# Kernel optimization log

Measured on AMD Instinct MI355X. Metric: run time of the kernel, lower is better.

The kernel has to match this reference:

```python
import jax, jax.numpy as jnp
import numpy as np

T, B, D, H = 32, 128, 256, 768
MAX_PONDER = 8
EPS = 0.01


def setup_inputs() -> dict:
    key = jax.random.key(0)
    ks = jax.random.split(key, 6)
    s = 1.0 / np.sqrt(H)
    return {
        "input_": jax.random.normal(ks[0], (T, B, D), jnp.float32),
        "W_ih": jax.random.uniform(ks[1], (H, D + 1), jnp.float32, -s, s),
        "W_hh": jax.random.uniform(ks[2], (H, H), jnp.float32, -s, s),
        "b_ih": jax.random.uniform(ks[3], (H,), jnp.float32, -s, s),
        "b_hh": jax.random.uniform(ks[4], (H,), jnp.float32, -s, s),
        "w_p": jax.random.uniform(ks[5], (H,), jnp.float32, -s, s),
        "b_p": jnp.ones((1,), jnp.float32),  # torch reset_parameters fills ponder bias with 1
    }


def reference(input_, W_ih, W_hh, b_ih, b_hh, w_p, b_p):
    T_, B_, D_ = input_.shape
    H_ = W_hh.shape[0]
    dt = input_.dtype
    hx0 = jnp.zeros((B_, H_), dt)

    def time_step(carry, x_t):
        hx, pcost = carry

        def ponder(c, _):
            hx_i, ah, ahx, sc, spc, mask, flag = c
            # input row with ponder flag (0 on first act step, 1 afterwards)
            x_in = jnp.concatenate([x_t, jnp.full((B_, 1), flag, dt)], axis=1)
            # ponder cost assigned for active rows before update
            spc = jnp.where(mask, -ah, spc)
            hx_new = jnp.tanh(x_in @ W_ih.T + b_ih + hx_i @ W_hh.T + b_hh)
            hx_i = jnp.where(mask[:, None], hx_new, hx_i)
            mf = mask.astype(dt)
            ahx = ahx + mf[:, None] * hx_new  # accum_hx += hx (as in source)
            h = jax.nn.sigmoid(hx_new @ w_p + b_p[0])
            ah2 = ah + mf * h
            p = h - jnp.maximum(ah2 - 1.0, 0.0)
            ahx = ahx + (mf * p)[:, None] * hx_new  # accum_hx += p*hx
            sc = sc + mf
            mask2 = ah2 < (1.0 - EPS)
            return (hx_i, ah2, ahx, sc, spc, mask2, jnp.ones((), dt)), None

        init = (hx,
                jnp.zeros((B_,), dt),           # accum_h
                jnp.zeros((B_, H_), dt),        # accum_hx
                jnp.zeros((B_,), dt),           # step_count
                jnp.zeros((B_,), dt),           # step_ponder_cost
                jnp.ones((B_,), bool),          # selector
                jnp.zeros((), dt))              # flag
        (hx_i, ah, ahx, sc, spc, mask, flag), _ = jax.lax.scan(
            ponder, init, None, length=MAX_PONDER)
        hx_out = ahx / sc[:, None]
        return (hx_out, pcost + spc), (hx_out, sc)

    (hx_last, pcost), (all_hx, steps) = jax.lax.scan(
        time_step, (hx0, jnp.zeros((B_,), dt)), input_)
    # all_hx: [T,B,H], hx: [1,B,H], ponder_cost: [B], ponder_times: [T,B]
    return all_hx, hx_last[None], pcost, steps
```

## Files before the change

### kernel.cpp

```cpp
#include <hip/hip_runtime.h>
#include <math.h>

#define TT 32
#define BB 128
#define DD 256
#define HH 768
#define MAXP 8

#define RG   8
#define RPG  16
#define CB   12
#define CS   64
#define NTH  256
#define NCH  24

#define OFF_LAST  ((size_t)TT * BB * HH)
#define OFF_PCOST (OFF_LAST + (size_t)BB * HH)
#define OFF_STEPS (OFF_PCOST + BB)

#define ASCOPE __HIP_MEMORY_SCOPE_AGENT

typedef __attribute__((ext_vector_type(8))) short s16x8;
typedef __attribute__((ext_vector_type(4))) float f32x4;
typedef unsigned long long ull;

static __device__ __forceinline__ unsigned short f2bf(float f) {
    unsigned u = __float_as_uint(f);
    u = (u + 0x7fffu + ((u >> 16) & 1u)) >> 16;
    return (unsigned short)u;
}
static __device__ __forceinline__ float bf2f(unsigned short h) {
    return __uint_as_float(((unsigned)h) << 16);
}

__launch_bounds__(NTH, 1)
__global__ void act_kernel(const float* __restrict__ x,
                           const float* __restrict__ Wih,
                           const float* __restrict__ Whh,
                           const float* __restrict__ bih,
                           const float* __restrict__ bhh,
                           const float* __restrict__ wpv,
                           const float* __restrict__ bp,
                           float* __restrict__ out,
                           unsigned* __restrict__ flags,
                           ull* __restrict__ hxe)
{
    const int tid  = threadIdx.x;
    const int g    = blockIdx.x & 7;
    const int ib   = blockIdx.x >> 3;
    const int r0   = g * RPG;
    const int c0   = ib * CS;
    const int CT   = tid >> 6;
    const int lane = tid & 63;
    const int am   = lane & 15;
    const int aq   = lane >> 4;

    __shared__ s16x8 A_s[NCH * 64];
    __shared__ s16x8 WB_s[4 * 8 * 64];
    __shared__ s16x8 xA_s[8 * 64];
    __shared__ unsigned short hxn_s[RPG][72];
    __shared__ float zw_s[4][20];
    __shared__ float bias_s[CS], wflag_s[CS];

    s16x8 Breg[NCH];
    {
        const float* wr = Whh + (size_t)(c0 + CT*16 + am) * HH + aq*8;
        for (int ch = 0; ch < NCH; ++ch) {
            float4 a0 = *(const float4*)(wr + ch*32);
            float4 a1 = *(const float4*)(wr + ch*32 + 4);
            union { s16x8 v; unsigned short e[8]; } u;
            u.e[0]=f2bf(a0.x); u.e[1]=f2bf(a0.y); u.e[2]=f2bf(a0.z); u.e[3]=f2bf(a0.w);
            u.e[4]=f2bf(a1.x); u.e[5]=f2bf(a1.y); u.e[6]=f2bf(a1.z); u.e[7]=f2bf(a1.w);
            Breg[ch] = u.v;
        }
    }
    for (int ch = 0; ch < 8; ++ch) {
        const float* wr = Wih + (size_t)(c0 + CT*16 + am) * (DD+1) + ch*32 + aq*8;
        union { s16x8 v; unsigned short e[8]; } u;
        #pragma unroll
        for (int j = 0; j < 8; ++j) u.e[j] = f2bf(wr[j]);
        WB_s[(CT*8 + ch)*64 + lane] = u.v;
    }
    if (tid < CS) {
        bias_s[tid]  = bih[c0+tid] + bhh[c0+tid];
        wflag_s[tid] = Wih[(size_t)(c0+tid)*(DD+1) + DD];
    }
    const float bpr = bp[0];
    float wpreg[48];
    #pragma unroll
    for (int j = 0; j < 6; ++j)
        #pragma unroll
        for (int i = 0; i < 8; ++i)
            wpreg[j*8+i] = wpv[(j*4 + CT)*32 + aq*8 + i];
    {
        s16x8 z8 = {0,0,0,0,0,0,0,0};
        #pragma unroll
        for (int j = 0; j < 6; ++j) A_s[j*NTH + tid] = z8;
    }

    float ahx[48];
    unsigned it = 0;
    float ahR = 0.f, spcR = 0.f, scR = 0.f, pcR = 0.f;
    int   actR = 1;

    float4 xp0, xp1, xp2, xp3;
    {
        const float* xb = x + (size_t)(r0 + am)*DD;
        xp0 = *(const float4*)(xb + CT*32 + aq*8);
        xp1 = *(const float4*)(xb + CT*32 + aq*8 + 4);
        xp2 = *(const float4*)(xb + (4+CT)*32 + aq*8);
        xp3 = *(const float4*)(xb + (4+CT)*32 + aq*8 + 4);
    }
    __syncthreads();

    for (int t = 0; t < TT; ++t) {
        {
            union { s16x8 v; unsigned short e[8]; } u;
            u.e[0]=f2bf(xp0.x); u.e[1]=f2bf(xp0.y); u.e[2]=f2bf(xp0.z); u.e[3]=f2bf(xp0.w);
            u.e[4]=f2bf(xp1.x); u.e[5]=f2bf(xp1.y); u.e[6]=f2bf(xp1.z); u.e[7]=f2bf(xp1.w);
            xA_s[tid] = u.v;
            u.e[0]=f2bf(xp2.x); u.e[1]=f2bf(xp2.y); u.e[2]=f2bf(xp2.z); u.e[3]=f2bf(xp2.w);
            u.e[4]=f2bf(xp3.x); u.e[5]=f2bf(xp3.y); u.e[6]=f2bf(xp3.z); u.e[7]=f2bf(xp3.w);
            xA_s[NTH + tid] = u.v;
        }
        ahR = 0.f; spcR = 0.f; scR = 0.f; actR = 1;
        #pragma unroll
        for (int q = 0; q < 48; ++q) ahx[q] = 0.f;
        __syncthreads();

        f32x4 xi;
        {
            f32x4 a0 = {0.f,0.f,0.f,0.f}, a1 = {0.f,0.f,0.f,0.f};
            #pragma unroll
            for (int ch = 0; ch < 8; ch += 2) {
                a0 = __builtin_amdgcn_mfma_f32_16x16x32_bf16(
                        xA_s[ch*64 + lane],     WB_s[(CT*8 + ch)*64 + lane],     a0, 0,0,0);
                a1 = __builtin_amdgcn_mfma_f32_16x16x32_bf16(
                        xA_s[(ch+1)*64 + lane], WB_s[(CT*8 + ch+1)*64 + lane],   a1, 0,0,0);
            }
            const float bs = bias_s[CT*16 + am];
            xi[0]=a0[0]+a1[0]+bs; xi[1]=a0[1]+a1[1]+bs;
            xi[2]=a0[2]+a1[2]+bs; xi[3]=a0[3]+a1[3]+bs;
        }
        if (t + 1 < TT) {
            const float* xb = x + ((size_t)(t+1)*BB + r0 + am)*DD;
            xp0 = *(const float4*)(xb + CT*32 + aq*8);
            xp1 = *(const float4*)(xb + CT*32 + aq*8 + 4);
            xp2 = *(const float4*)(xb + (4+CT)*32 + aq*8);
            xp3 = *(const float4*)(xb + (4+CT)*32 + aq*8 + 4);
        }

        int pk = 0;
        for (;;) {
            const unsigned par = it & 1u;
            ull* exch = hxe + (size_t)(g*2 + par) * (NCH*64*2);

            f32x4 a0 = xi, a1 = {0.f,0.f,0.f,0.f};
            #pragma unroll
            for (int ch = 0; ch < NCH; ch += 2) {
                a0 = __builtin_amdgcn_mfma_f32_16x16x32_bf16(A_s[ch*64 + lane],     Breg[ch],   a0, 0,0,0);
                a1 = __builtin_amdgcn_mfma_f32_16x16x32_bf16(A_s[(ch+1)*64 + lane], Breg[ch+1], a1, 0,0,0);
            }
            const float fl = pk ? wflag_s[CT*16 + am] : 0.f;
            #pragma unroll
            for (int r = 0; r < 4; ++r)
                hxn_s[aq*4 + r][CT*16 + am] = f2bf(tanhf(a0[r] + a1[r] + fl));
            __syncthreads();

            {
                const int u4  = tid >> 6, l = tid & 63;
                const int chd = u4 >> 1, half = u4 & 1;
                const int pm  = l & 15, pq = l >> 4;
                const ull v = *(const ull*)&hxn_s[pm][chd*32 + pq*8 + half*4];
                __hip_atomic_store(exch + ((size_t)((2*ib + chd)*64 + l)*2 + half),
                                   v, __ATOMIC_RELAXED, ASCOPE);
            }
            ++it;
            __syncthreads();
            if (tid == 0)
                __hip_atomic_store(&flags[g*16 + ib], it, __ATOMIC_RELEASE, ASCOPE);
            if (tid < 64) {
                const unsigned* fa = &flags[g*16 + (tid % 12)];
                unsigned v;
                do { v = __hip_atomic_load(fa, __ATOMIC_RELAXED, ASCOPE); }
                while (!__all((int)(v >= it)));
                __builtin_amdgcn_fence(__ATOMIC_ACQUIRE, "agent");
            }
            __syncthreads();

            ull nlo[6], nhi[6];
            #pragma unroll
            for (int j = 0; j < 6; ++j) {
                ull* src = exch + (size_t)(j*NTH + tid)*2;
                nlo[j] = __hip_atomic_load(src,     __ATOMIC_RELAXED, ASCOPE);
                nhi[j] = __hip_atomic_load(src + 1, __ATOMIC_RELAXED, ASCOPE);
            }

            float zp = 0.f;
            #pragma unroll
            for (int j = 0; j < 6; ++j) {
                const ull lo = nlo[j], hi = nhi[j];
                #pragma unroll
                for (int i = 0; i < 4; ++i) {
                    zp += bf2f((unsigned short)(lo >> (16*i))) * wpreg[j*8 + i];
                    zp += bf2f((unsigned short)(hi >> (16*i))) * wpreg[j*8 + 4 + i];
                }
            }
            zp += __shfl_xor(zp, 16);
            zp += __shfl_xor(zp, 32);
            if (lane < 16) zw_s[CT][lane] = zp;
            __syncthreads();
            const float z = ((zw_s[0][am] + zw_s[1][am]) + zw_s[2][am]) + zw_s[3][am];

            float w1 = 0.f;
            if (actR) {
                const float h = 1.f / (1.f + expf(-(z + bpr)));
                spcR = -ahR;
                const float ah2 = ahR + h;
                const float p = h - fmaxf(ah2 - 1.f, 0.f);
                w1 = 1.f + p;
                scR += 1.f;
                ahR = ah2;
                actR = (ah2 < 0.99f) ? 1 : 0;
            }

            if (w1 != 0.f) {
                #pragma unroll
                for (int j = 0; j < 6; ++j) {
                    const ull lo = nlo[j], hi = nhi[j];
                    #pragma unroll
                    for (int i = 0; i < 4; ++i) {
                        ahx[j*8 + i]     += w1 * bf2f((unsigned short)(lo >> (16*i)));
                        ahx[j*8 + 4 + i] += w1 * bf2f((unsigned short)(hi >> (16*i)));
                    }
                    union { ull u[2]; s16x8 v; } cv; cv.u[0] = lo; cv.u[1] = hi;
                    A_s[j*NTH + tid] = cv.v;
                }
            }
            const int nact = (int)__popcll(__ballot(actR != 0) & 0xFFFFull);
            ++pk;
            __syncthreads();
            if (nact == 0 || pk == MAXP) break;
        }

        pcR += spcR;
        const float inv = 1.f / scR;
        if (ib == 0 && tid < 16) out[OFF_STEPS + (size_t)t*BB + r0 + tid] = scR;
        #pragma unroll
        for (int j = 0; j < 6; ++j) {
            float o[8];
            #pragma unroll
            for (int i = 0; i < 8; ++i) o[i] = ahx[j*8 + i] * inv;
            union { s16x8 v; unsigned short e[8]; } u;
            #pragma unroll
            for (int i = 0; i < 8; ++i) u.e[i] = f2bf(o[i]);
            A_s[j*NTH + tid] = u.v;
            if (ib == 0) {
                float* op = out + ((size_t)t*BB + r0 + am)*HH + (j*4 + CT)*32 + aq*8;
                *(float4*)op       = make_float4(o[0], o[1], o[2], o[3]);
                *(float4*)(op + 4) = make_float4(o[4], o[5], o[6], o[7]);
                if (t == TT-1) {
                    float* lp = out + OFF_LAST + (size_t)(r0 + am)*HH + (j*4 + CT)*32 + aq*8;
                    *(float4*)lp       = make_float4(o[0], o[1], o[2], o[3]);
                    *(float4*)(lp + 4) = make_float4(o[4], o[5], o[6], o[7]);
                }
            }
        }
        __syncthreads();
    }
    if (ib == 0 && tid < 16) out[OFF_PCOST + r0 + tid] = pcR;
}

extern "C" void kernel_launch(void* const* d_in, const int* in_sizes, int n_in,
                              void* d_out, int out_size, void* d_ws, size_t ws_size,
                              hipStream_t stream) {
    const float* x   = (const float*)d_in[0];
    const float* Wih = (const float*)d_in[1];
    const float* Whh = (const float*)d_in[2];
    const float* bih = (const float*)d_in[3];
    const float* bhh = (const float*)d_in[4];
    const float* wpv = (const float*)d_in[5];
    const float* bp  = (const float*)d_in[6];
    float* out = (float*)d_out;

    unsigned* flags = (unsigned*)d_ws;
    ull*      hxe   = (ull*)((char*)d_ws + 4096);

    hipMemsetAsync(d_ws, 0, 4096, stream);
    act_kernel<<<dim3(RG*CB), dim3(NTH), 0, stream>>>(
        x, Wih, Whh, bih, bhh, wpv, bp, out, flags, hxe);
}
```

Baseline: 406.1 us.

## Replace flag barrier with sequence-tagged exchange words for inter-block hidden-state sync

Each 64-bit exchange word now carries three bf16 values plus a 16-bit sequence tag, so consumers poll the data directly until every tag matches the current iteration. This removes the separate release-flag store, the flag spin-wait and a block barrier from every ponder step. A lagging progress counter, checked two iterations back, protects the double-buffered slots from being overwritten early. The cost is 33% more exchange traffic, wider polling loads, and a larger workspace memset.

```diff
diff --git a/kernel.cpp b/kernel.cpp
--- a/kernel.cpp
+++ b/kernel.cpp
@@ -19,6 +19,8 @@
 #define OFF_STEPS (OFF_PCOST + BB)
 
 #define ASCOPE __HIP_MEMORY_SCOPE_AGENT
+
+#define BUF_ULL (RPG * 96 * 3)
 
 typedef __attribute__((ext_vector_type(8))) short s16x8;
 typedef __attribute__((ext_vector_type(4))) float f32x4;
@@ -42,7 +44,7 @@
                            const float* __restrict__ wpv,
                            const float* __restrict__ bp,
                            float* __restrict__ out,
-                           unsigned* __restrict__ flags,
+                           unsigned* __restrict__ progress,
                            ull* __restrict__ hxe)
 {
     const int tid  = threadIdx.x;
@@ -99,9 +101,12 @@
     }
 
     float ahx[48];
-    unsigned it = 0;
+    unsigned it = 1;
     float ahR = 0.f, spcR = 0.f, scR = 0.f, pcR = 0.f;
     int   actR = 1;
+
+    const int wr_r = tid >> 3;
+    const int wr_o = tid & 7;
 
     float4 xp0, xp1, xp2, xp3;
     {
@@ -152,8 +157,9 @@
 
         int pk = 0;
         for (;;) {
-            const unsigned par = it & 1u;
-            ull* exch = hxe + (size_t)(g*2 + par) * (NCH*64*2);
+            const unsigned cur = it;
+            const ull sq = (ull)(cur & 0xffffu);
+            ull* exch = hxe + (size_t)(g*2 + (cur & 1u)) * BUF_ULL;
 
             f32x4 a0 = xi, a1 = {0.f,0.f,0.f,0.f};
             #pragma unroll
@@ -167,49 +173,70 @@
                 hxn_s[aq*4 + r][CT*16 + am] = f2bf(tanhf(a0[r] + a1[r] + fl));
             __syncthreads();
 
+            if (cur > 2) {
+                const unsigned tgt = cur - 2;
+                const unsigned* pa = &progress[g*16 + (lane % 12)];
+                unsigned v;
+                do { v = __hip_atomic_load(pa, __ATOMIC_RELAXED, ASCOPE); }
+                while (!__all((int)(v >= tgt)));
+            }
+
+            if (tid < 128) {
+                const ull A = *(const ull*)&hxn_s[wr_r][wr_o*8];
+                const ull B = *(const ull*)&hxn_s[wr_r][wr_o*8 + 4];
+                const ull u0 = (A & 0x0000FFFFFFFFFFFFULL) | (sq << 48);
+                const ull u1 = ((A >> 48) | ((B & 0xFFFFFFFFULL) << 16)) | (sq << 48);
+                const ull u2 = (B >> 32) | (sq << 48);
+                ull* dst = exch + (size_t)(wr_r*96 + ib*8 + wr_o)*3;
+                __hip_atomic_store(dst,     u0, __ATOMIC_RELAXED, ASCOPE);
+                __hip_atomic_store(dst + 1, u1, __ATOMIC_RELAXED, ASCOPE);
+                __hip_atomic_store(dst + 2, u2, __ATOMIC_RELAXED, ASCOPE);
+            }
+
+            ull u0[6], u1[6], u2[6];
             {
-                const int u4  = tid >> 6, l = tid & 63;
-                const int chd = u4 >> 1, half = u4 & 1;
-                const int pm  = l & 15, pq = l >> 4;
-                const ull v = *(const ull*)&hxn_s[pm][chd*32 + pq*8 + half*4];
-                __hip_atomic_store(exch + ((size_t)((2*ib + chd)*64 + l)*2 + half),
-                                   v, __ATOMIC_RELAXED, ASCOPE);
-            }
-            ++it;
-            __syncthreads();
-            if (tid == 0)
-                __hip_atomic_store(&flags[g*16 + ib], it, __ATOMIC_RELEASE, ASCOPE);
-            if (tid < 64) {
-                const unsigned* fa = &flags[g*16 + (tid % 12)];
-                unsigned v;
-                do { v = __hip_atomic_load(fa, __ATOMIC_RELAXED, ASCOPE); }
-                while (!__all((int)(v >= it)));
-                __builtin_amdgcn_fence(__ATOMIC_ACQUIRE, "agent");
-            }
-            __syncthreads();
-
-            ull nlo[6], nhi[6];
+                const ull* bptr[6];
+                #pragma unroll
+                for (int j = 0; j < 6; ++j)
+                    bptr[j] = exch + (size_t)(am*96 + ((j*4 + CT)*4 + aq))*3;
+                int okall;
+                do {
+                    okall = 1;
+                    #pragma unroll
+                    for (int j = 0; j < 6; ++j) {
+                        u0[j] = __hip_atomic_load(bptr[j],     __ATOMIC_RELAXED, ASCOPE);
+                        u1[j] = __hip_atomic_load(bptr[j] + 1, __ATOMIC_RELAXED, ASCOPE);
+                        u2[j] = __hip_atomic_load(bptr[j] + 2, __ATOMIC_RELAXED, ASCOPE);
+                    }
+                    #pragma unroll
+                    for (int j = 0; j < 6; ++j)
+                        okall &= ((u0[j] >> 48) == sq) & ((u1[j] >> 48) == sq)
+                               & ((u2[j] >> 48) == sq);
+                } while (!__all(okall));
+            }
+
+            unsigned short d[48];
             #pragma unroll
             for (int j = 0; j < 6; ++j) {
-                ull* src = exch + (size_t)(j*NTH + tid)*2;
-                nlo[j] = __hip_atomic_load(src,     __ATOMIC_RELAXED, ASCOPE);
-                nhi[j] = __hip_atomic_load(src + 1, __ATOMIC_RELAXED, ASCOPE);
+                d[j*8+0] = (unsigned short)u0[j];
+                d[j*8+1] = (unsigned short)(u0[j] >> 16);
+                d[j*8+2] = (unsigned short)(u0[j] >> 32);
+                d[j*8+3] = (unsigned short)u1[j];
+                d[j*8+4] = (unsigned short)(u1[j] >> 16);
+                d[j*8+5] = (unsigned short)(u1[j] >> 32);
+                d[j*8+6] = (unsigned short)u2[j];
+                d[j*8+7] = (unsigned short)(u2[j] >> 16);
             }
 
             float zp = 0.f;
             #pragma unroll
-            for (int j = 0; j < 6; ++j) {
-                const ull lo = nlo[j], hi = nhi[j];
-                #pragma unroll
-                for (int i = 0; i < 4; ++i) {
-                    zp += bf2f((unsigned short)(lo >> (16*i))) * wpreg[j*8 + i];
-                    zp += bf2f((unsigned short)(hi >> (16*i))) * wpreg[j*8 + 4 + i];
-                }
-            }
+            for (int q = 0; q < 48; ++q) zp += bf2f(d[q]) * wpreg[q];
             zp += __shfl_xor(zp, 16);
             zp += __shfl_xor(zp, 32);
             if (lane < 16) zw_s[CT][lane] = zp;
             __syncthreads();
+            if (tid == 0)
+                __hip_atomic_store(&progress[g*16 + ib], cur, __ATOMIC_RELAXED, ASCOPE);
             const float z = ((zw_s[0][am] + zw_s[1][am]) + zw_s[2][am]) + zw_s[3][am];
 
             float w1 = 0.f;
@@ -227,18 +254,17 @@
             if (w1 != 0.f) {
                 #pragma unroll
                 for (int j = 0; j < 6; ++j) {
-                    const ull lo = nlo[j], hi = nhi[j];
+                    union { s16x8 v; unsigned short e[8]; } cv;
                     #pragma unroll
-                    for (int i = 0; i < 4; ++i) {
-                        ahx[j*8 + i]     += w1 * bf2f((unsigned short)(lo >> (16*i)));
-                        ahx[j*8 + 4 + i] += w1 * bf2f((unsigned short)(hi >> (16*i)));
+                    for (int i = 0; i < 8; ++i) {
+                        ahx[j*8 + i] += w1 * bf2f(d[j*8 + i]);
+                        cv.e[i] = d[j*8 + i];
                     }
-                    union { ull u[2]; s16x8 v; } cv; cv.u[0] = lo; cv.u[1] = hi;
                     A_s[j*NTH + tid] = cv.v;
                 }
             }
             const int nact = (int)__popcll(__ballot(actR != 0) & 0xFFFFull);
-            ++pk;
+            ++it; ++pk;
             __syncthreads();
             if (nact == 0 || pk == MAXP) break;
         }
@@ -283,10 +309,11 @@
     const float* bp  = (const float*)d_in[6];
     float* out = (float*)d_out;
 
-    unsigned* flags = (unsigned*)d_ws;
-    ull*      hxe   = (ull*)((char*)d_ws + 4096);
-
-    hipMemsetAsync(d_ws, 0, 4096, stream);
+    unsigned* progress = (unsigned*)d_ws;
+    ull*      hxe      = (ull*)((char*)d_ws + 4096);
+    const size_t clr = 4096 + (size_t)RG * 2 * BUF_ULL * 8;
+
+    hipMemsetAsync(d_ws, 0, clr, stream);
     act_kernel<<<dim3(RG*CB), dim3(NTH), 0, stream>>>(
-        x, Wih, Whh, bih, bhh, wpv, bp, out, flags, hxe);
+        x, Wih, Whh, bih, bhh, wpv, bp, out, progress, hxe);
 }
```

After: 679.0 us. +67.2%, slower.
